# Kernel optimization log

Hardware: AMD Instinct MI355X
Metric: run time of the kernel (lower is better)

## Reference

```python
import jax, jax.numpy as jnp
import numpy as np

BATCH = 65536
T = 500
IN_DIM = 2
HID = 64        # ODEFunc hidden_dim
G_HID = 52      # CNN (control) hidden dim


def setup_inputs() -> dict:
    key = jax.random.key(0)
    ks = jax.random.split(key, 14)
    s = 0.1  # small init scale keeps the 500-step Euler rollout numerically tame
    inp = {
        "y0": jax.random.normal(ks[0], (BATCH, IN_DIM), dtype=jnp.float32),
        "t": (jnp.arange(T, dtype=jnp.float32) * 0.01),
        # ODEFunc: Linear(2,64) -> Tanh -> Linear(64,64) -> Softplus -> Linear(64,2)
        "f_w1": jax.random.normal(ks[1], (HID, IN_DIM), dtype=jnp.float32) * s,
        "f_b1": jax.random.normal(ks[2], (HID,), dtype=jnp.float32) * s,
        "f_w2": jax.random.normal(ks[3], (HID, HID), dtype=jnp.float32) * s,
        "f_b2": jax.random.normal(ks[4], (HID,), dtype=jnp.float32) * s,
        "f_w3": jax.random.normal(ks[5], (IN_DIM, HID), dtype=jnp.float32) * s,
        "f_b3": jax.random.normal(ks[6], (IN_DIM,), dtype=jnp.float32) * s,
        # CNN g: Conv1d(2,52,k=1) -> Tanh -> Conv1d(52,52,k=1) -> Softplus -> Conv1d(52,2,k=1)
        # kernel_size=1 conv on a length-1 sequence == Linear, so store as [out,in] matrices
        "g_w1": jax.random.normal(ks[7], (G_HID, IN_DIM), dtype=jnp.float32) * s,
        "g_b1": jax.random.normal(ks[8], (G_HID,), dtype=jnp.float32) * s,
        "g_w2": jax.random.normal(ks[9], (G_HID, G_HID), dtype=jnp.float32) * s,
        "g_b2": jax.random.normal(ks[10], (G_HID,), dtype=jnp.float32) * s,
        "g_w3": jax.random.normal(ks[11], (IN_DIM, G_HID), dtype=jnp.float32) * s,
        "g_b3": jax.random.normal(ks[12], (IN_DIM,), dtype=jnp.float32) * s,
    }
    return inp


def _mlp(y, w1, b1, w2, b2, w3, b3):
    # Linear -> Tanh -> Linear -> Softplus -> Linear (matches both ODEFunc and
    # the kernel_size=1 CNN, which is mathematically identical to an MLP)
    h = jnp.tanh(y @ w1.T + b1)
    h = jax.nn.softplus(h @ w2.T + b2)
    return h @ w3.T + b3


def reference(y0, t, f_w1, f_b1, f_w2, f_b2, f_w3, f_b3,
              g_w1, g_b1, g_w2, g_b2, g_w3, g_b3):
    dt = t[1] - t[0]  # euler_ode_solver uses a fixed dt from the first interval

    def step(y, _):
        u = _mlp(y, g_w1, g_b1, g_w2, g_b2, g_w3, g_b3)       # control g(y)
        f = _mlp(y, f_w1, f_b1, f_w2, f_b2, f_w3, f_b3)       # func(t, y)
        y_next = y + (f + u) * dt
        return y_next, y_next

    _, ys = jax.lax.scan(step, y0, None, length=t.shape[0] - 1)
    return jnp.concatenate([y0[None], ys], axis=0)  # [T, batch, input_dim]
```

## Files before the change

### kernel.cpp

```cpp
#include <hip/hip_runtime.h>

#define BATCH 65536
#define T 500

typedef __attribute__((ext_vector_type(8))) short bf16x8;
typedef __attribute__((ext_vector_type(4))) float f32x4;

#define MFMA(A, B, C) __builtin_amdgcn_mfma_f32_16x16x32_bf16(A, B, C, 0, 0, 0)
#define PSEL 0x07060302u

#define LOG2E 1.44269504088896340736f
#define LN2   0.693147180559945309417f

union U4 { unsigned u[4]; bf16x8 v; };

__device__ __forceinline__ float exp2_fast(float x) {
#if __has_builtin(__builtin_amdgcn_exp2f)
    return __builtin_amdgcn_exp2f(x);
#else
    float r; asm("v_exp_f32 %0, %1" : "=v"(r) : "v"(x)); return r;
#endif
}
__device__ __forceinline__ float log2_fast(float x) {
#if __has_builtin(__builtin_amdgcn_logf)
    return __builtin_amdgcn_logf(x);
#else
    float r; asm("v_log_f32 %0, %1" : "=v"(r) : "v"(x)); return r;
#endif
}

__device__ __forceinline__ float tanh_act(float d) {
    return 1.0f - 2.0f * __builtin_amdgcn_rcpf(exp2_fast(d) + 1.0f);
}
__device__ __forceinline__ float sp_act(float d) {
    return log2_fast(exp2_fast(d) + 1.0f);
}

__device__ __forceinline__ void tsplit(float x, short& hs, short& ls) {
    unsigned uh = __float_as_uint(x) & 0xFFFF0000u;
    float r = x - __uint_as_float(uh);
    hs = (short)(uh >> 16);
    ls = (short)(__float_as_uint(r) >> 16);
}

__device__ __forceinline__ void build_l1(const float* __restrict__ W,
                                         const float* __restrict__ Bv,
                                         int Mreal, int t, int lane, float scale,
                                         bf16x8& A) {
    int row = t * 16 + (lane & 15);
    int G = lane >> 4;
    float wa = 0.f, wb = 0.f, bi = 0.f;
    if (row < Mreal) {
        wa = W[2 * row] * scale;
        wb = W[2 * row + 1] * scale;
        bi = Bv[row] * scale;
    }
    short wah, wal, wbh, wbl, bih, bil;
    tsplit(wa, wah, wal);
    tsplit(wb, wbh, wbl);
    tsplit(bi, bih, bil);
    #pragma unroll
    for (int j = 0; j < 8; ++j) A[j] = 0;
    if (G == 0) {
        A[0] = wah; A[1] = wbh; A[2] = bih; A[3] = wah;
        A[4] = wbh; A[5] = wah; A[6] = wbh; A[7] = wal;
    } else if (G == 1) {
        A[0] = wbl; A[1] = wal; A[2] = wbl; A[3] = bil;
    }
}

__device__ __forceinline__ void build_frag_pi(const float* __restrict__ W,
                                              int Mreal, int Kreal, int Ks,
                                              int t, int u, int lane, float scale,
                                              bf16x8& hi, bf16x8& lo) {
    int row = t * 16 + (lane & 15);
    int G = lane >> 4;
    #pragma unroll
    for (int j = 0; j < 8; ++j) {
        int hidden = 16 * (2 * u + (j >> 2)) + 4 * G + (j & 3);
        float w = (row < Mreal && hidden < Kreal) ? W[row * Ks + hidden] * scale : 0.0f;
        short hs, ls;
        tsplit(w, hs, ls);
        hi[j] = hs; lo[j] = ls;
    }
}

template<bool TANH>
__device__ __forceinline__ U4 act_pack2(f32x4 dA, f32x4 dB) {
    float a0 = TANH ? tanh_act(dA[0]) : sp_act(dA[0]);
    float a1 = TANH ? tanh_act(dA[1]) : sp_act(dA[1]);
    float a2 = TANH ? tanh_act(dA[2]) : sp_act(dA[2]);
    float a3 = TANH ? tanh_act(dA[3]) : sp_act(dA[3]);
    float b0 = TANH ? tanh_act(dB[0]) : sp_act(dB[0]);
    float b1 = TANH ? tanh_act(dB[1]) : sp_act(dB[1]);
    float b2 = TANH ? tanh_act(dB[2]) : sp_act(dB[2]);
    float b3 = TANH ? tanh_act(dB[3]) : sp_act(dB[3]);
    U4 r;
    r.u[0] = __builtin_amdgcn_perm(__float_as_uint(a1), __float_as_uint(a0), PSEL);
    r.u[1] = __builtin_amdgcn_perm(__float_as_uint(a3), __float_as_uint(a2), PSEL);
    r.u[2] = __builtin_amdgcn_perm(__float_as_uint(b1), __float_as_uint(b0), PSEL);
    r.u[3] = __builtin_amdgcn_perm(__float_as_uint(b3), __float_as_uint(b2), PSEL);
    return r;
}

__device__ __forceinline__ void build_yB(float ya, float yb, int G, U4& yB) {
    unsigned ua = __float_as_uint(ya), ub = __float_as_uint(yb);
    unsigned uah = ua & 0xFFFF0000u;
    float ra = ya - __uint_as_float(uah);
    unsigned uam = __float_as_uint(ra) & 0xFFFF0000u;
    float ra2 = ra - __uint_as_float(uam);
    unsigned ubh = ub & 0xFFFF0000u;
    float rb = yb - __uint_as_float(ubh);
    unsigned ubm = __float_as_uint(rb) & 0xFFFF0000u;
    float rb2 = rb - __uint_as_float(ubm);

    unsigned w0g0 = __builtin_amdgcn_perm(ub, ua, PSEL);
    unsigned w1g0 = 0x00003F80u | uam;
    unsigned w2g0 = __builtin_amdgcn_perm(__float_as_uint(ra2), __float_as_uint(rb), PSEL);
    unsigned w3g0 = __builtin_amdgcn_perm(ua, __float_as_uint(rb2), PSEL);
    unsigned w0g1 = __builtin_amdgcn_perm(__float_as_uint(ra), ub, PSEL);
    unsigned w1g1 = (ubm >> 16) | 0x3F800000u;

    yB.u[0] = (G == 0) ? w0g0 : ((G == 1) ? w0g1 : 0u);
    yB.u[1] = (G == 0) ? w1g0 : ((G == 1) ? w1g1 : 0u);
    yB.u[2] = (G == 0) ? w2g0 : 0u;
    yB.u[3] = (G == 0) ? w3g0 : 0u;
}

__global__ void __launch_bounds__(512)
__attribute__((amdgpu_waves_per_eu(4, 4)))
node_kernel(const float* __restrict__ y0,
            const float* __restrict__ tt,
            const float* __restrict__ fw1, const float* __restrict__ fb1,
            const float* __restrict__ fw2, const float* __restrict__ fb2,
            const float* __restrict__ fw3, const float* __restrict__ fb3,
            const float* __restrict__ gw1, const float* __restrict__ gb1,
            const float* __restrict__ gw2, const float* __restrict__ gb2,
            const float* __restrict__ gw3, const float* __restrict__ gb3,
            float* __restrict__ out)
{
    __shared__ float lds_y[8][16][2];
    __shared__ __align__(16) float lds_b2[2][64];
    __shared__ __align__(16) unsigned lds_l1[2][4][256];
    __shared__ __align__(16) unsigned lds_w2h[2][8][256];
    __shared__ __align__(16) unsigned lds_w2l[2][8][256];
    __shared__ __align__(16) unsigned lds_w3A[2][2][256];

    const int lane  = threadIdx.x & 63;
    const int wIdx  = threadIdx.x >> 6;
    const int waveG = blockIdx.x * 8 + wIdx;
    const int c     = lane & 15;
    const int G     = lane >> 4;
    const bool lo16 = (lane < 16);
    const int lane4 = lane * 4;

    if (threadIdx.x < 64) {
        int i = threadIdx.x;
        lds_b2[0][i] = fb2[i] * LOG2E;
        lds_b2[1][i] = (i < 52) ? gb2[i] * LOG2E : 0.0f;
    }

    if (wIdx < 4) {
        const int t = wIdx;
        bf16x8 A, hi, lo;
        build_l1(fw1, fb1, 64, t, lane, 2.0f * LOG2E, A);
        *reinterpret_cast<bf16x8*>(&lds_l1[0][t][lane4]) = A;
        build_l1(gw1, gb1, 52, t, lane, 2.0f * LOG2E, A);
        *reinterpret_cast<bf16x8*>(&lds_l1[1][t][lane4]) = A;
        #pragma unroll
        for (int u = 0; u < 2; ++u) {
            build_frag_pi(fw2, 64, 64, 64, t, u, lane, LOG2E, hi, lo);
            *reinterpret_cast<bf16x8*>(&lds_w2h[0][2 * t + u][lane4]) = hi;
            *reinterpret_cast<bf16x8*>(&lds_w2l[0][2 * t + u][lane4]) = lo;
            build_frag_pi(gw2, 52, 52, 52, t, u, lane, LOG2E, hi, lo);
            *reinterpret_cast<bf16x8*>(&lds_w2h[1][2 * t + u][lane4]) = hi;
            *reinterpret_cast<bf16x8*>(&lds_w2l[1][2 * t + u][lane4]) = lo;
        }
    } else {
        const int net = (wIdx - 4) >> 1;
        const int u   = (wIdx - 4) & 1;
        bf16x8 hi, lo;
        build_frag_pi(net ? gw3 : fw3, 2, net ? 52 : 64, net ? 52 : 64,
                      0, u, lane, LN2, hi, lo);
        *reinterpret_cast<bf16x8*>(&lds_w3A[net][u][lane4]) = hi;
    }
    __syncthreads();

    const float dt = tt[1] - tt[0];
    const float b3a = fb3[0] + gb3[0];
    const float b3b = fb3[1] + gb3[1];
    const f32x4 zero4 = {0.f, 0.f, 0.f, 0.f};

    {
        int sample = waveG * 16 + c;
        if (lo16) {
            float2 yv = reinterpret_cast<const float2*>(y0)[sample];
            lds_y[wIdx][c][0] = yv.x;
            lds_y[wIdx][c][1] = yv.y;
            reinterpret_cast<float2*>(out)[sample] = yv;
        }
    }

    #pragma unroll 1
    for (int s = 1; s < T; ++s) {
        unsigned zoff = 0;
        asm volatile("" : "+v"(zoff));
        const unsigned z4 = zoff << 2;

        float ya = lds_y[wIdx][c][0];
        float yb = lds_y[wIdx][c][1];

        U4 yB;
        build_yB(ya, yb, G, yB);

        f32x4 acc3;
        acc3[0] = lo16 ? b3a : 0.f;
        acc3[1] = lo16 ? b3b : 0.f;
        acc3[2] = 0.f;
        acc3[3] = 0.f;

        #pragma unroll
        for (int net = 0; net < 2; ++net) {
            f32x4 d0, d1, d2, d3;
            {
                bf16x8 A0 = *reinterpret_cast<const bf16x8*>(&lds_l1[net][0][lane4 + z4]);
                bf16x8 A1 = *reinterpret_cast<const bf16x8*>(&lds_l1[net][1][lane4 + z4]);
                bf16x8 A2 = *reinterpret_cast<const bf16x8*>(&lds_l1[net][2][lane4 + z4]);
                bf16x8 A3 = *reinterpret_cast<const bf16x8*>(&lds_l1[net][3][lane4 + z4]);
                d0 = MFMA(A0, yB.v, zero4);
                d1 = MFMA(A1, yB.v, zero4);
                d2 = MFMA(A2, yB.v, zero4);
                d3 = MFMA(A3, yB.v, zero4);
            }
            U4 H0 = act_pack2<true>(d0, d1);
            U4 H1 = act_pack2<true>(d2, d3);

            #pragma unroll
            for (int half = 0; half < 2; ++half) {
                f32x4 e[2];
                #pragma unroll
                for (int k = 0; k < 2; ++k) {
                    int t = 2 * half + k;
                    f32x4 a = *reinterpret_cast<const f32x4*>(&lds_b2[net][16 * t + 4 * G + z4]);
                    #pragma unroll
                    for (int u = 0; u < 2; ++u) {
                        bf16x8 wh = *reinterpret_cast<const bf16x8*>(&lds_w2h[net][2 * t + u][lane4 + z4]);
                        bf16x8 wl = *reinterpret_cast<const bf16x8*>(&lds_w2l[net][2 * t + u][lane4 + z4]);
                        a = MFMA(wh, u ? H1.v : H0.v, a);
                        a = MFMA(wl, u ? H1.v : H0.v, a);
                    }
                    e[k] = a;
                }
                U4 S = act_pack2<false>(e[0], e[1]);
                bf16x8 w3f = *reinterpret_cast<const bf16x8*>(&lds_w3A[net][half][lane4 + z4]);
                acc3 = MFMA(w3f, S.v, acc3);
            }
        }

        if (lo16) {
            float nya = fmaf(acc3[0], dt, ya);
            float nyb = fmaf(acc3[1], dt, yb);
            lds_y[wIdx][c][0] = nya;
            lds_y[wIdx][c][1] = nyb;
            int sample = waveG * 16 + c;
            reinterpret_cast<float2*>(out)[(size_t)s * BATCH + sample] =
                make_float2(nya, nyb);
        }
    }
}

extern "C" void kernel_launch(void* const* d_in, const int* in_sizes, int n_in,
                              void* d_out, int out_size, void* d_ws, size_t ws_size,
                              hipStream_t stream) {
    const float* y0  = (const float*)d_in[0];
    const float* tt  = (const float*)d_in[1];
    const float* fw1 = (const float*)d_in[2];
    const float* fb1 = (const float*)d_in[3];
    const float* fw2 = (const float*)d_in[4];
    const float* fb2 = (const float*)d_in[5];
    const float* fw3 = (const float*)d_in[6];
    const float* fb3 = (const float*)d_in[7];
    const float* gw1 = (const float*)d_in[8];
    const float* gb1 = (const float*)d_in[9];
    const float* gw2 = (const float*)d_in[10];
    const float* gb2 = (const float*)d_in[11];
    const float* gw3 = (const float*)d_in[12];
    const float* gb3 = (const float*)d_in[13];
    float* out = (float*)d_out;

    dim3 grid(512);
    dim3 block(512);
    hipLaunchKernelGGL(node_kernel, grid, block, 0, stream,
                       y0, tt, fw1, fb1, fw2, fb2, fw3, fb3,
                       gw1, gb1, gw2, gb2, gw3, gb3, out);
}
```

Before: 1.914 ms.

## Drop third bf16 split term in layer-1 and keep state in registers via shuffles

Layer-1 input emulation moves from a three-term bf16 split of y and the weights to a two-term hi/lo split. This drops the G==1 lane group's MFMA contribution and several split and perm ops per step. The per-wave y state no longer goes through LDS each step: every lane holds y in registers and a cross-lane shuffle broadcasts the updated value from the first 16 lanes. The cost is lower accuracy in the first-layer product, which could matter over a 500-step Euler rollout.

```diff
diff --git a/kernel.cpp b/kernel.cpp
--- a/kernel.cpp
+++ b/kernel.cpp
@@ -63,9 +63,7 @@
     for (int j = 0; j < 8; ++j) A[j] = 0;
     if (G == 0) {
         A[0] = wah; A[1] = wbh; A[2] = bih; A[3] = wah;
-        A[4] = wbh; A[5] = wah; A[6] = wbh; A[7] = wal;
-    } else if (G == 1) {
-        A[0] = wbl; A[1] = wal; A[2] = wbl; A[3] = bil;
+        A[4] = wbh; A[5] = wal; A[6] = wbl; A[7] = bil;
     }
 }
 
@@ -107,24 +105,19 @@
     unsigned ua = __float_as_uint(ya), ub = __float_as_uint(yb);
     unsigned uah = ua & 0xFFFF0000u;
     float ra = ya - __uint_as_float(uah);
-    unsigned uam = __float_as_uint(ra) & 0xFFFF0000u;
-    float ra2 = ra - __uint_as_float(uam);
     unsigned ubh = ub & 0xFFFF0000u;
     float rb = yb - __uint_as_float(ubh);
-    unsigned ubm = __float_as_uint(rb) & 0xFFFF0000u;
-    float rb2 = rb - __uint_as_float(ubm);
-
-    unsigned w0g0 = __builtin_amdgcn_perm(ub, ua, PSEL);
-    unsigned w1g0 = 0x00003F80u | uam;
-    unsigned w2g0 = __builtin_amdgcn_perm(__float_as_uint(ra2), __float_as_uint(rb), PSEL);
-    unsigned w3g0 = __builtin_amdgcn_perm(ua, __float_as_uint(rb2), PSEL);
-    unsigned w0g1 = __builtin_amdgcn_perm(__float_as_uint(ra), ub, PSEL);
-    unsigned w1g1 = (ubm >> 16) | 0x3F800000u;
-
-    yB.u[0] = (G == 0) ? w0g0 : ((G == 1) ? w0g1 : 0u);
-    yB.u[1] = (G == 0) ? w1g0 : ((G == 1) ? w1g1 : 0u);
-    yB.u[2] = (G == 0) ? w2g0 : 0u;
-    yB.u[3] = (G == 0) ? w3g0 : 0u;
+
+    unsigned w0 = __builtin_amdgcn_perm(ub, ua, PSEL);
+    unsigned w1 = 0x00003F80u | (__float_as_uint(ra) & 0xFFFF0000u);
+    unsigned w2 = __builtin_amdgcn_perm(ua, __float_as_uint(rb), PSEL);
+    unsigned w3 = (ubh >> 16) | 0x3F800000u;
+
+    bool g0 = (G == 0);
+    yB.u[0] = g0 ? w0 : 0u;
+    yB.u[1] = g0 ? w1 : 0u;
+    yB.u[2] = g0 ? w2 : 0u;
+    yB.u[3] = g0 ? w3 : 0u;
 }
 
 __global__ void __launch_bounds__(512)
@@ -139,7 +132,6 @@
             const float* __restrict__ gw3, const float* __restrict__ gb3,
             float* __restrict__ out)
 {
-    __shared__ float lds_y[8][16][2];
     __shared__ __align__(16) float lds_b2[2][64];
     __shared__ __align__(16) unsigned lds_l1[2][4][256];
     __shared__ __align__(16) unsigned lds_w2h[2][8][256];
@@ -191,14 +183,12 @@
     const float b3b = fb3[1] + gb3[1];
     const f32x4 zero4 = {0.f, 0.f, 0.f, 0.f};
 
+    float ya, yb;
     {
         int sample = waveG * 16 + c;
-        if (lo16) {
-            float2 yv = reinterpret_cast<const float2*>(y0)[sample];
-            lds_y[wIdx][c][0] = yv.x;
-            lds_y[wIdx][c][1] = yv.y;
-            reinterpret_cast<float2*>(out)[sample] = yv;
-        }
+        float2 yv = reinterpret_cast<const float2*>(y0)[sample];
+        ya = yv.x; yb = yv.y;
+        if (lo16) reinterpret_cast<float2*>(out)[sample] = yv;
     }
 
     #pragma unroll 1
@@ -206,9 +196,6 @@
         unsigned zoff = 0;
         asm volatile("" : "+v"(zoff));
         const unsigned z4 = zoff << 2;
-
-        float ya = lds_y[wIdx][c][0];
-        float yb = lds_y[wIdx][c][1];
 
         U4 yB;
         build_yB(ya, yb, G, yB);
@@ -257,15 +244,15 @@
             }
         }
 
+        float nya = fmaf(acc3[0], dt, ya);
+        float nyb = fmaf(acc3[1], dt, yb);
         if (lo16) {
-            float nya = fmaf(acc3[0], dt, ya);
-            float nyb = fmaf(acc3[1], dt, yb);
-            lds_y[wIdx][c][0] = nya;
-            lds_y[wIdx][c][1] = nyb;
             int sample = waveG * 16 + c;
             reinterpret_cast<float2*>(out)[(size_t)s * BATCH + sample] =
                 make_float2(nya, nyb);
         }
+        ya = __shfl(nya, c);
+        yb = __shfl(nyb, c);
     }
 }
 
```

Measured after the change: 1.878 ms. About the same (-1.9%).
